# Kernel optimization log

Hardware: AMD Instinct MI355X
Metric: run time of the kernel (lower is better)

The kernel has to match this reference:

```python
import jax, jax.numpy as jnp
import numpy as np

VOCAB, EMB, HID, OUT = 4411, 64, 128, 2


def setup_inputs() -> dict:
    key = jax.random.key(0)
    ks = jax.random.split(key, 8)
    inputs = jax.random.randint(ks[0], (1024, 512), 0, VOCAB)
    s_e = 1.0
    s_ih = 1.0 / np.sqrt(HID)
    emb_table = jax.random.normal(ks[1], (VOCAB, EMB), dtype=jnp.float32) * s_e
    W_ih = jax.random.uniform(ks[2], (HID, EMB), dtype=jnp.float32, minval=-s_ih, maxval=s_ih)
    W_hh = jax.random.uniform(ks[3], (HID, HID), dtype=jnp.float32, minval=-s_ih, maxval=s_ih)
    b_ih = jax.random.uniform(ks[4], (HID,), dtype=jnp.float32, minval=-s_ih, maxval=s_ih)
    b_hh = jax.random.uniform(ks[5], (HID,), dtype=jnp.float32, minval=-s_ih, maxval=s_ih)
    s_l = 1.0 / np.sqrt(HID)
    W_lin = jax.random.uniform(ks[6], (OUT, HID), dtype=jnp.float32, minval=-s_l, maxval=s_l)
    b_lin = jax.random.uniform(ks[7], (OUT,), dtype=jnp.float32, minval=-s_l, maxval=s_l)
    return {"inputs": inputs, "emb_table": emb_table, "W_ih": W_ih, "W_hh": W_hh,
            "b_ih": b_ih, "b_hh": b_hh, "W_lin": W_lin, "b_lin": b_lin}


def reference(inputs, emb_table, W_ih, W_hh, b_ih, b_hh, W_lin, b_lin):
    # Embedding lookup: [B, T, EMB]
    emb = emb_table[inputs]
    B = emb.shape[0]
    # Precompute input projection for all timesteps: [B, T, HID]
    x_proj = jnp.einsum('bte,he->bth', emb, W_ih) + b_ih + b_hh
    h0 = jnp.zeros((B, W_hh.shape[0]), dtype=emb.dtype)

    def step(h, x_t):  # x_t: [B, HID]
        h_new = jnp.tanh(x_t + h @ W_hh.T)
        return h_new, None

    # scan over time axis
    h_final, _ = jax.lax.scan(step, h0, jnp.swapaxes(x_proj, 0, 1))
    # out_state squeeze(dim=0) -> [B, HID]; linear head -> [B, 2]
    return h_final @ W_lin.T + b_lin
```

## Files before the change

### kernel.cpp

```cpp
#include <hip/hip_runtime.h>
#include <hip/hip_bf16.h>


constexpr int Bc    = 1024;
constexpr int Tc    = 512;
constexpr int Ec    = 64;
constexpr int Hc    = 128;
constexpr int OUTc  = 2;
constexpr int VOCAB = 4411;

typedef int   intx4  __attribute__((ext_vector_type(4)));
typedef float floatx4 __attribute__((ext_vector_type(4)));

#define LGKM_BARRIER() asm volatile("s_waitcnt lgkmcnt(0)\n\ts_barrier" ::: "memory")

__device__ __forceinline__ int pack4i8(int i0, int i1, int i2, int i3) {
    return (i0 & 255) | ((i1 & 255) << 8) | ((i2 & 255) << 16) | ((i3 & 255) << 24);
}
__device__ __forceinline__ int tanh127(float z) {
    const float e = __builtin_amdgcn_exp2f(2.8853900817779268f * z);
    const float r = __builtin_amdgcn_rcpf(e + 1.0f);
    return __float2int_rn(fmaf(-254.0f, r, 127.0f));
}

constexpr int PV = 16;
__global__ __launch_bounds__(256) void pe_kernel(
    const float* __restrict__ emb, const float* __restrict__ W_ih,
    const float* __restrict__ b_ih, const float* __restrict__ b_hh,
    float* __restrict__ pe)
{
    const int tid  = threadIdx.x;
    const int j    = tid & 127;
    const int half = tid >> 7;
    const int v0   = blockIdx.x * PV;

    __shared__ float es[PV * Ec];
    for (int i = tid; i < PV * Ec / 4; i += 256) {
        const int flat = i * 4, vv = flat >> 6;
        if (v0 + vv < VOCAB)
            *(float4*)&es[flat] = *(const float4*)(emb + (long)(v0 + vv) * Ec + (flat & 63));
    }

    float4 wr[Ec / 4];
#pragma unroll
    for (int e = 0; e < Ec / 4; ++e)
        wr[e] = *(const float4*)(W_ih + j * Ec + e * 4);
    const float bias = b_ih[j] + b_hh[j];

    __syncthreads();

    const int vbeg = half * (PV / 2), vend = vbeg + PV / 2;
    for (int vv = vbeg; vv < vend; ++vv) {
        if (v0 + vv >= VOCAB) break;
        const float* er = &es[vv * Ec];
        float a0 = bias, a1 = 0.f, a2 = 0.f, a3 = 0.f;
#pragma unroll
        for (int e = 0; e < Ec / 4; ++e) {
            const float4 E = *(const float4*)(er + 4 * e);
            a0 = fmaf(E.x, wr[e].x, a0);
            a1 = fmaf(E.y, wr[e].y, a1);
            a2 = fmaf(E.z, wr[e].z, a2);
            a3 = fmaf(E.w, wr[e].w, a3);
        }
        pe[(long)(v0 + vv) * Hc + j] = (a0 + a1) + (a2 + a3);
    }
}

constexpr int HT_BUF     = 2048;
constexpr int TOK_STRIDE = 513;

__global__ __attribute__((amdgpu_flat_work_group_size(512, 512)))
void rnn_mfma(
    const int*   __restrict__ inputs,
    const float* __restrict__ pe,
    const float* __restrict__ W_hh,
    const float* __restrict__ W_lin,
    const float* __restrict__ b_lin,
    float* __restrict__ out)
{
    const int tid = threadIdx.x;
    const int w   = tid >> 6;
    const int L   = tid & 63;
    const int q   = L >> 4;
    const int b   = L & 15;
    const int blk = blockIdx.x;
    const int jb  = w * 16;

    __shared__ __align__(16) signed char HT[2 * HT_BUF];
    __shared__ int toks[16 * TOK_STRIDE];

    {
        const int base = blk * 16 * Tc;
        for (int i = tid; i < 16 * Tc / 4; i += 512) {
            const int4 v4 = *(const int4*)(inputs + base + i * 4);
            const int bb = (i * 4) >> 9, t0 = (i * 4) & 511;
            int* dst = &toks[bb * TOK_STRIDE + t0];
            dst[0] = v4.x; dst[1] = v4.y; dst[2] = v4.z; dst[3] = v4.w;
        }
    }
    {
        unsigned int* z = (unsigned int*)HT;
        for (int i = tid; i < HT_BUF / 4; i += 512) z[i] = 0u;
    }

    const float s_W  = 127.0f * 11.313708498984761f;
    const float invs = 1.0f / (127.0f * 127.0f * 11.313708498984761f);
    intx4 wfrag[2];
    {
        const float* wr = W_hh + (jb + b) * Hc;
#pragma unroll
        for (int kt = 0; kt < 2; ++kt) {
#pragma unroll
            for (int d = 0; d < 4; ++d) {
                const float4 v = *(const float4*)(wr + kt * 64 + q * 16 + d * 4);
                wfrag[kt][d] = pack4i8(__float2int_rn(v.x * s_W),
                                       __float2int_rn(v.y * s_W),
                                       __float2int_rn(v.z * s_W),
                                       __float2int_rn(v.w * s_W));
            }
        }
    }
    asm volatile("" : "+v"(wfrag[0]), "+v"(wfrag[1]));

    signed char* const ht0 = HT;
    signed char* const ht1 = HT + HT_BUF;
    const int rd_base = L * 16;
    const int wr_off = ((w >> 2) << 10) + (((w & 3) * 16 + b) << 4) + q * 4;
    const int xp_off = jb + q * 4;

    const int* tr = &toks[b * TOK_STRIDE];
    const intx4 zac = (intx4){0, 0, 0, 0};

    __syncthreads();

    float4 xpc, xpn;
    {
        const int t0 = tr[0], t1 = tr[1];
        xpc = *(const float4*)(pe + (long)t0 * Hc + xp_off);
        xpn = *(const float4*)(pe + (long)t1 * Hc + xp_off);
    }

    for (int t = 0; t < Tc; ++t) {
        signed char* const rbuf = (t & 1) ? ht1 : ht0;
        signed char* const wbuf = (t & 1) ? ht0 : ht1;

        intx4 bfrag[2];
#pragma unroll
        for (int kt = 0; kt < 2; ++kt)
            bfrag[kt] = *(const intx4*)(rbuf + kt * 1024 + rd_base);

        float4 xp2;
        {
            const int tk = tr[(t + 2 < Tc) ? (t + 2) : (Tc - 1)];
            xp2 = *(const float4*)(pe + (long)tk * Hc + xp_off);
        }

        intx4 acc = __builtin_amdgcn_mfma_i32_16x16x64_i8(wfrag[0], bfrag[0], zac, 0, 0, 0);
        acc = __builtin_amdgcn_mfma_i32_16x16x64_i8(wfrag[1], bfrag[1], acc, 0, 0, 0);

        const int i0 = tanh127(fmaf((float)acc[0], invs, xpc.x));
        const int i1 = tanh127(fmaf((float)acc[1], invs, xpc.y));
        const int i2 = tanh127(fmaf((float)acc[2], invs, xpc.z));
        const int i3 = tanh127(fmaf((float)acc[3], invs, xpc.w));
        *(int*)(wbuf + wr_off) = pack4i8(i0, i1, i2, i3);

        LGKM_BARRIER();

        xpc = xpn;
        xpn = xp2;
    }

    if (tid < 16 * OUTc) {
        const int bb = tid >> 1, o = tid & 1;
        float s = b_lin[o];
        const float* wl = W_lin + o * Hc;
        const float ih = 1.0f / 127.0f;
#pragma unroll 8
        for (int k = 0; k < Hc; ++k) {
            const int off = ((k >> 6) << 10) + ((((k >> 4) & 3) * 16 + bb) << 4) + (k & 15);
            s = fmaf((float)ht0[off] * ih, wl[k], s);
        }
        out[(blk * 16 + bb) * OUTc + o] = s;
    }
}

extern "C" void kernel_launch(void* const* d_in, const int* in_sizes, int n_in,
                              void* d_out, int out_size, void* d_ws, size_t ws_size,
                              hipStream_t stream) {
    const int*   inputs    = (const int*)d_in[0];
    const float* emb_table = (const float*)d_in[1];
    const float* W_ih      = (const float*)d_in[2];
    const float* W_hh      = (const float*)d_in[3];
    const float* b_ih      = (const float*)d_in[4];
    const float* b_hh      = (const float*)d_in[5];
    const float* W_lin     = (const float*)d_in[6];
    const float* b_lin     = (const float*)d_in[7];
    float* out = (float*)d_out;

    float* pe = (float*)d_ws;
    pe_kernel<<<(VOCAB + PV - 1) / PV, 256, 0, stream>>>(emb_table, W_ih, b_ih, b_hh, pe);
    rnn_mfma<<<Bc / 16, 512, 0, stream>>>(inputs, pe, W_hh, W_lin, b_lin, out);
}
```

Baseline: 238.3 us.

## Halve RNN block to four waves with two MFMA tiles each, fold projection into accumulator

The recurrent kernel now runs 256 threads per block, each wave computing two 16-row output tiles, so each per-step barrier synchronises fewer waves. The input projection is prequantized to int32 at the accumulator scale and fed as the MFMA C operand. This removes the per-element float FMA before tanh and lets the scale fold into the exp2 argument. The cost is more serial MFMA and tanh work per wave each step, plus extra int32 rounding of the projection.

```diff
diff --git a/kernel.cpp b/kernel.cpp
--- a/kernel.cpp
+++ b/kernel.cpp
@@ -10,15 +10,17 @@
 constexpr int VOCAB = 4411;
 
 typedef int   intx4  __attribute__((ext_vector_type(4)));
-typedef float floatx4 __attribute__((ext_vector_type(4)));
+
+#define S_SCALE 182458.08595437f
+#define KINV    (2.8853900817779268f / S_SCALE)
 
 #define LGKM_BARRIER() asm volatile("s_waitcnt lgkmcnt(0)\n\ts_barrier" ::: "memory")
 
 __device__ __forceinline__ int pack4i8(int i0, int i1, int i2, int i3) {
     return (i0 & 255) | ((i1 & 255) << 8) | ((i2 & 255) << 16) | ((i3 & 255) << 24);
 }
-__device__ __forceinline__ int tanh127(float z) {
-    const float e = __builtin_amdgcn_exp2f(2.8853900817779268f * z);
+__device__ __forceinline__ int tanh127i(float accf) {
+    const float e = __builtin_amdgcn_exp2f(KINV * accf);
     const float r = __builtin_amdgcn_rcpf(e + 1.0f);
     return __float2int_rn(fmaf(-254.0f, r, 127.0f));
 }
@@ -27,7 +29,7 @@
 __global__ __launch_bounds__(256) void pe_kernel(
     const float* __restrict__ emb, const float* __restrict__ W_ih,
     const float* __restrict__ b_ih, const float* __restrict__ b_hh,
-    float* __restrict__ pe)
+    int* __restrict__ pei)
 {
     const int tid  = threadIdx.x;
     const int j    = tid & 127;
@@ -62,17 +64,18 @@
             a2 = fmaf(E.z, wr[e].z, a2);
             a3 = fmaf(E.w, wr[e].w, a3);
         }
-        pe[(long)(v0 + vv) * Hc + j] = (a0 + a1) + (a2 + a3);
+        pei[(long)(v0 + vv) * Hc + j] =
+            __float2int_rn(((a0 + a1) + (a2 + a3)) * S_SCALE);
     }
 }
 
 constexpr int HT_BUF     = 2048;
 constexpr int TOK_STRIDE = 513;
 
-__global__ __attribute__((amdgpu_flat_work_group_size(512, 512)))
+__global__ __attribute__((amdgpu_flat_work_group_size(256, 256)))
 void rnn_mfma(
     const int*   __restrict__ inputs,
-    const float* __restrict__ pe,
+    const int*   __restrict__ pei,
     const float* __restrict__ W_hh,
     const float* __restrict__ W_lin,
     const float* __restrict__ b_lin,
@@ -84,14 +87,14 @@
     const int q   = L >> 4;
     const int b   = L & 15;
     const int blk = blockIdx.x;
-    const int jb  = w * 16;
+    const int jb  = w * 32;
 
     __shared__ __align__(16) signed char HT[2 * HT_BUF];
     __shared__ int toks[16 * TOK_STRIDE];
 
     {
         const int base = blk * 16 * Tc;
-        for (int i = tid; i < 16 * Tc / 4; i += 512) {
+        for (int i = tid; i < 16 * Tc / 4; i += 256) {
             const int4 v4 = *(const int4*)(inputs + base + i * 4);
             const int bb = (i * 4) >> 9, t0 = (i * 4) & 511;
             int* dst = &toks[bb * TOK_STRIDE + t0];
@@ -100,44 +103,51 @@
     }
     {
         unsigned int* z = (unsigned int*)HT;
-        for (int i = tid; i < HT_BUF / 4; i += 512) z[i] = 0u;
-    }
-
-    const float s_W  = 127.0f * 11.313708498984761f;
-    const float invs = 1.0f / (127.0f * 127.0f * 11.313708498984761f);
-    intx4 wfrag[2];
-    {
-        const float* wr = W_hh + (jb + b) * Hc;
+        for (int i = tid; i < HT_BUF / 4; i += 256) z[i] = 0u;
+    }
+
+    const float s_W = 127.0f * 11.313708498984761f;
+    intx4 wfrag[2][2];
+#pragma unroll
+    for (int mt = 0; mt < 2; ++mt) {
+        const float* wr = W_hh + (jb + mt * 16 + b) * Hc;
 #pragma unroll
         for (int kt = 0; kt < 2; ++kt) {
 #pragma unroll
             for (int d = 0; d < 4; ++d) {
                 const float4 v = *(const float4*)(wr + kt * 64 + q * 16 + d * 4);
-                wfrag[kt][d] = pack4i8(__float2int_rn(v.x * s_W),
-                                       __float2int_rn(v.y * s_W),
-                                       __float2int_rn(v.z * s_W),
-                                       __float2int_rn(v.w * s_W));
+                wfrag[mt][kt][d] = pack4i8(__float2int_rn(v.x * s_W),
+                                           __float2int_rn(v.y * s_W),
+                                           __float2int_rn(v.z * s_W),
+                                           __float2int_rn(v.w * s_W));
             }
         }
     }
-    asm volatile("" : "+v"(wfrag[0]), "+v"(wfrag[1]));
+    asm volatile("" : "+v"(wfrag[0][0]), "+v"(wfrag[0][1]),
+                      "+v"(wfrag[1][0]), "+v"(wfrag[1][1]));
 
     signed char* const ht0 = HT;
     signed char* const ht1 = HT + HT_BUF;
     const int rd_base = L * 16;
-    const int wr_off = ((w >> 2) << 10) + (((w & 3) * 16 + b) << 4) + q * 4;
+    int wr_off[2];
+#pragma unroll
+    for (int mt = 0; mt < 2; ++mt) {
+        const int j0 = jb + mt * 16 + q * 4;
+        wr_off[mt] = ((j0 >> 6) << 10) + ((((j0 >> 4) & 3) * 16 + b) << 4) + (j0 & 15);
+    }
     const int xp_off = jb + q * 4;
 
     const int* tr = &toks[b * TOK_STRIDE];
-    const intx4 zac = (intx4){0, 0, 0, 0};
 
     __syncthreads();
 
-    float4 xpc, xpn;
+    int4 xpc0, xpc1, xpn0, xpn1;
     {
         const int t0 = tr[0], t1 = tr[1];
-        xpc = *(const float4*)(pe + (long)t0 * Hc + xp_off);
-        xpn = *(const float4*)(pe + (long)t1 * Hc + xp_off);
+        xpc0 = *(const int4*)(pei + (long)t0 * Hc + xp_off);
+        xpc1 = *(const int4*)(pei + (long)t0 * Hc + xp_off + 16);
+        xpn0 = *(const int4*)(pei + (long)t1 * Hc + xp_off);
+        xpn1 = *(const int4*)(pei + (long)t1 * Hc + xp_off + 16);
     }
 
     for (int t = 0; t < Tc; ++t) {
@@ -149,25 +159,34 @@
         for (int kt = 0; kt < 2; ++kt)
             bfrag[kt] = *(const intx4*)(rbuf + kt * 1024 + rd_base);
 
-        float4 xp2;
+        int4 xf0, xf1;
         {
             const int tk = tr[(t + 2 < Tc) ? (t + 2) : (Tc - 1)];
-            xp2 = *(const float4*)(pe + (long)tk * Hc + xp_off);
-        }
-
-        intx4 acc = __builtin_amdgcn_mfma_i32_16x16x64_i8(wfrag[0], bfrag[0], zac, 0, 0, 0);
-        acc = __builtin_amdgcn_mfma_i32_16x16x64_i8(wfrag[1], bfrag[1], acc, 0, 0, 0);
-
-        const int i0 = tanh127(fmaf((float)acc[0], invs, xpc.x));
-        const int i1 = tanh127(fmaf((float)acc[1], invs, xpc.y));
-        const int i2 = tanh127(fmaf((float)acc[2], invs, xpc.z));
-        const int i3 = tanh127(fmaf((float)acc[3], invs, xpc.w));
-        *(int*)(wbuf + wr_off) = pack4i8(i0, i1, i2, i3);
+            const int* p = pei + (long)tk * Hc + xp_off;
+            xf0 = *(const int4*)(p);
+            xf1 = *(const int4*)(p + 16);
+        }
+
+        const intx4 c0 = (intx4){xpc0.x, xpc0.y, xpc0.z, xpc0.w};
+        const intx4 c1 = (intx4){xpc1.x, xpc1.y, xpc1.z, xpc1.w};
+        intx4 a0 = __builtin_amdgcn_mfma_i32_16x16x64_i8(wfrag[0][0], bfrag[0], c0, 0, 0, 0);
+        intx4 a1 = __builtin_amdgcn_mfma_i32_16x16x64_i8(wfrag[1][0], bfrag[0], c1, 0, 0, 0);
+        a0 = __builtin_amdgcn_mfma_i32_16x16x64_i8(wfrag[0][1], bfrag[1], a0, 0, 0, 0);
+        a1 = __builtin_amdgcn_mfma_i32_16x16x64_i8(wfrag[1][1], bfrag[1], a1, 0, 0, 0);
+
+        *(int*)(wbuf + wr_off[0]) = pack4i8(tanh127i((float)a0[0]),
+                                            tanh127i((float)a0[1]),
+                                            tanh127i((float)a0[2]),
+                                            tanh127i((float)a0[3]));
+        *(int*)(wbuf + wr_off[1]) = pack4i8(tanh127i((float)a1[0]),
+                                            tanh127i((float)a1[1]),
+                                            tanh127i((float)a1[2]),
+                                            tanh127i((float)a1[3]));
 
         LGKM_BARRIER();
 
-        xpc = xpn;
-        xpn = xp2;
+        xpc0 = xpn0; xpc1 = xpn1;
+        xpn0 = xf0;  xpn1 = xf1;
     }
 
     if (tid < 16 * OUTc) {
@@ -197,7 +216,7 @@
     const float* b_lin     = (const float*)d_in[7];
     float* out = (float*)d_out;
 
-    float* pe = (float*)d_ws;
-    pe_kernel<<<(VOCAB + PV - 1) / PV, 256, 0, stream>>>(emb_table, W_ih, b_ih, b_hh, pe);
-    rnn_mfma<<<Bc / 16, 512, 0, stream>>>(inputs, pe, W_hh, W_lin, b_lin, out);
-}
+    int* pei = (int*)d_ws;
+    pe_kernel<<<(VOCAB + PV - 1) / PV, 256, 0, stream>>>(emb_table, W_ih, b_ih, b_hh, pei);
+    rnn_mfma<<<Bc / 16, 256, 0, stream>>>(inputs, pei, W_hh, W_lin, b_lin, out);
+}
```

New measurement: 289.2 us. 21.4% more time.

## Fuse embedding projection into RNN kernel with flag-based grid barrier

Applied to the files above, without the earlier changes.

Removes the separate pe_kernel launch. Each of the 64 RNN blocks now computes a slice of the vocabulary's input projection table, publishes a per-block ready flag and spins until all blocks are done before starting the recurrence. This saves a kernel launch and the gap between the two kernels. In exchange it adds a cross-block spin barrier, relies on all blocks being resident at once, and stores the flags in the tail of the output buffer without resetting them between calls, which is fragile.

```diff
diff --git a/kernel.cpp b/kernel.cpp
--- a/kernel.cpp
+++ b/kernel.cpp
@@ -8,9 +8,10 @@
 constexpr int Hc    = 128;
 constexpr int OUTc  = 2;
 constexpr int VOCAB = 4411;
-
-typedef int   intx4  __attribute__((ext_vector_type(4)));
-typedef float floatx4 __attribute__((ext_vector_type(4)));
+constexpr int NBLK  = Bc / 16;
+constexpr int PVB   = (VOCAB + NBLK - 1) / NBLK;
+
+typedef int intx4 __attribute__((ext_vector_type(4)));
 
 #define LGKM_BARRIER() asm volatile("s_waitcnt lgkmcnt(0)\n\ts_barrier" ::: "memory")
 
@@ -23,56 +24,17 @@
     return __float2int_rn(fmaf(-254.0f, r, 127.0f));
 }
 
-constexpr int PV = 16;
-__global__ __launch_bounds__(256) void pe_kernel(
-    const float* __restrict__ emb, const float* __restrict__ W_ih,
-    const float* __restrict__ b_ih, const float* __restrict__ b_hh,
-    float* __restrict__ pe)
-{
-    const int tid  = threadIdx.x;
-    const int j    = tid & 127;
-    const int half = tid >> 7;
-    const int v0   = blockIdx.x * PV;
-
-    __shared__ float es[PV * Ec];
-    for (int i = tid; i < PV * Ec / 4; i += 256) {
-        const int flat = i * 4, vv = flat >> 6;
-        if (v0 + vv < VOCAB)
-            *(float4*)&es[flat] = *(const float4*)(emb + (long)(v0 + vv) * Ec + (flat & 63));
-    }
-
-    float4 wr[Ec / 4];
-#pragma unroll
-    for (int e = 0; e < Ec / 4; ++e)
-        wr[e] = *(const float4*)(W_ih + j * Ec + e * 4);
-    const float bias = b_ih[j] + b_hh[j];
-
-    __syncthreads();
-
-    const int vbeg = half * (PV / 2), vend = vbeg + PV / 2;
-    for (int vv = vbeg; vv < vend; ++vv) {
-        if (v0 + vv >= VOCAB) break;
-        const float* er = &es[vv * Ec];
-        float a0 = bias, a1 = 0.f, a2 = 0.f, a3 = 0.f;
-#pragma unroll
-        for (int e = 0; e < Ec / 4; ++e) {
-            const float4 E = *(const float4*)(er + 4 * e);
-            a0 = fmaf(E.x, wr[e].x, a0);
-            a1 = fmaf(E.y, wr[e].y, a1);
-            a2 = fmaf(E.z, wr[e].z, a2);
-            a3 = fmaf(E.w, wr[e].w, a3);
-        }
-        pe[(long)(v0 + vv) * Hc + j] = (a0 + a1) + (a2 + a3);
-    }
-}
-
 constexpr int HT_BUF     = 2048;
 constexpr int TOK_STRIDE = 513;
 
 __global__ __attribute__((amdgpu_flat_work_group_size(512, 512)))
 void rnn_mfma(
     const int*   __restrict__ inputs,
-    const float* __restrict__ pe,
+    const float* __restrict__ emb,
+    const float* __restrict__ W_ih,
+    const float* __restrict__ b_ih,
+    const float* __restrict__ b_hh,
+    float*       __restrict__ pe,
     const float* __restrict__ W_hh,
     const float* __restrict__ W_lin,
     const float* __restrict__ b_lin,
@@ -86,6 +48,8 @@
     const int blk = blockIdx.x;
     const int jb  = w * 16;
 
+    int* const flags = (int*)out + Bc * OUTc - NBLK;
+
     __shared__ __align__(16) signed char HT[2 * HT_BUF];
     __shared__ int toks[16 * TOK_STRIDE];
 
@@ -101,6 +65,39 @@
     {
         unsigned int* z = (unsigned int*)HT;
         for (int i = tid; i < HT_BUF / 4; i += 512) z[i] = 0u;
+    }
+
+    {
+        const int j  = tid & 127;
+        const int g  = tid >> 7;
+        const int v0 = blk * PVB;
+
+        float4 wr[Ec / 4];
+#pragma unroll
+        for (int e = 0; e < Ec / 4; ++e)
+            wr[e] = *(const float4*)(W_ih + j * Ec + e * 4);
+        const float bias = b_ih[j] + b_hh[j];
+
+        for (int v = v0 + g; v < v0 + PVB && v < VOCAB; v += 4) {
+            const float* er = emb + (long)v * Ec;
+            float a0 = bias, a1 = 0.f, a2 = 0.f, a3 = 0.f;
+#pragma unroll
+            for (int e = 0; e < Ec / 4; ++e) {
+                const float4 E = *(const float4*)(er + 4 * e);
+                a0 = fmaf(E.x, wr[e].x, a0);
+                a1 = fmaf(E.y, wr[e].y, a1);
+                a2 = fmaf(E.z, wr[e].z, a2);
+                a3 = fmaf(E.w, wr[e].w, a3);
+            }
+            pe[(long)v * Hc + j] = (a0 + a1) + (a2 + a3);
+        }
+    }
+
+    __syncthreads();
+    if (tid == 0) {
+        __threadfence();
+        __hip_atomic_store(&flags[blk], 1, __ATOMIC_RELEASE,
+                           __HIP_MEMORY_SCOPE_AGENT);
     }
 
     const float s_W  = 127.0f * 11.313708498984761f;
@@ -131,6 +128,17 @@
     const int* tr = &toks[b * TOK_STRIDE];
     const intx4 zac = (intx4){0, 0, 0, 0};
 
+    if (tid == 0) {
+        int ready = 0;
+        while (ready != NBLK) {
+            ready = 0;
+            for (int i = 0; i < NBLK; ++i)
+                ready += (__hip_atomic_load(&flags[i], __ATOMIC_RELAXED,
+                                            __HIP_MEMORY_SCOPE_AGENT) == 1);
+            if (ready != NBLK) __builtin_amdgcn_s_sleep(8);
+        }
+        __threadfence();
+    }
     __syncthreads();
 
     float4 xpc, xpn;
@@ -198,6 +206,6 @@
     float* out = (float*)d_out;
 
     float* pe = (float*)d_ws;
-    pe_kernel<<<(VOCAB + PV - 1) / PV, 256, 0, stream>>>(emb_table, W_ih, b_ih, b_hh, pe);
-    rnn_mfma<<<Bc / 16, 512, 0, stream>>>(inputs, pe, W_hh, W_lin, b_lin, out);
-}
+    rnn_mfma<<<NBLK, 512, 0, stream>>>(inputs, emb_table, W_ih, b_ih, b_hh,
+                                       pe, W_hh, W_lin, b_lin, out);
+}
```

Result: slower. 264.5 us (+11.0%).
